# Kernel optimization log

Measured on AMD Instinct MI355X. Metric: run time of the kernel, lower is better.

The kernel has to match this reference:

```python
import jax, jax.numpy as jnp
import numpy as np

D_IN, D, H, NE, NPATCH, B = 768, 512, 4, 2048, 49, 512
DH = D // H


def _match(q, k, w, b):
    # q:[N,Lq,D], k:[N,Lk,D] -> cross-attention of q over k, then linear proj
    s = jnp.einsum('nqd,nkd->nqk', q, k) * (q.shape[-1] ** -0.5)
    a = jax.nn.softmax(s, axis=-1)
    return jnp.einsum('nqk,nkd->nqd', a, k) @ w + b


def _mh_pool(x, query, wq, bq, wk, bk, wv, bv, wo, bo):
    # multi-head attention pooling with 1 learned query -> [N, D]
    N, P, _ = x.shape
    q = (query @ wq + bq).reshape(H, 1, DH)                      # [H,1,dh]
    k = (x @ wk + bk).reshape(N, P, H, DH).transpose(0, 2, 1, 3)  # [N,H,P,dh]
    v = (x @ wv + bv).reshape(N, P, H, DH).transpose(0, 2, 1, 3)
    s = jnp.einsum('hqd,nhkd->nhqk', q, k) * (DH ** -0.5)
    a = jax.nn.softmax(s, axis=-1)
    o = jnp.einsum('nhqk,nhkd->nhqd', a, v).transpose(0, 2, 1, 3).reshape(N, D)
    return o @ wo + bo


def _ln(x, g, b):
    m = jnp.mean(x, -1, keepdims=True)
    v = jnp.var(x, -1, keepdims=True)
    return (x - m) * jax.lax.rsqrt(v + 1e-5) * g + b


def _moe(t, i, gw, gb, tw1, tb1, tw2, tb2, iw1, ib1, iw2, ib2):
    # 2-expert softmax-gated combiner over (text, pooled image) features
    gate = jax.nn.softmax(jnp.concatenate([t, i], -1) @ gw + gb, axis=-1)  # [N,2]
    et = jax.nn.relu(t @ tw1 + tb1) @ tw2 + tb2
    ei = jax.nn.relu(i @ iw1 + ib1) @ iw2 + ib2
    return gate[:, :1] * et + gate[:, 1:] * ei


def setup_inputs():
    key = jax.random.key(0)
    ks = jax.random.split(key, 24)
    g = lambda i, sh, s=0.02: jax.random.normal(ks[i], sh, dtype=jnp.float32) * s
    z = lambda *sh: jnp.zeros(sh, jnp.float32)
    return dict(
        entity_text_cls=g(0, (NE, D_IN), 1.0),
        entity_image_tokens=g(1, (NE, NPATCH, D_IN), 1.0),
        mention_text_cls=g(2, (B, D_IN), 1.0),
        mention_image_tokens=g(3, (B, NPATCH, D_IN), 1.0),
        text_fc_w=g(4, (D_IN, D)), text_fc_b=z(D),
        image_fc_w=g(5, (D_IN, D)), image_fc_b=z(D),
        gate_fc_w=g(6, (D, 1)), gate_fc_b=z(1),
        ln_g=jnp.ones((D,), jnp.float32), ln_b=z(D),
        match_w=g(7, (D, D)), match_b=z(D),
        mh_query=g(8, (1, D)),
        mh_wq=g(9, (D, D)), mh_bq=z(D),
        mh_wk=g(10, (D, D)), mh_bk=z(D),
        mh_wv=g(11, (D, D)), mh_bv=z(D),
        mh_wo=g(12, (D, D)), mh_bo=z(D),
        moe_gw=g(13, (2 * D, 2)), moe_gb=z(2),
        moe_tw1=g(14, (D, D)), moe_tb1=z(D),
        moe_tw2=g(15, (D, D)), moe_tb2=z(D),
        moe_iw1=g(16, (D, D)), moe_ib1=z(D),
        moe_iw2=g(17, (D, D)), moe_ib2=z(D),
    )


def reference(entity_text_cls, entity_image_tokens, mention_text_cls, mention_image_tokens,
              text_fc_w, text_fc_b, image_fc_w, image_fc_b, gate_fc_w, gate_fc_b,
              ln_g, ln_b, match_w, match_b, mh_query,
              mh_wq, mh_bq, mh_wk, mh_bk, mh_wv, mh_bv, mh_wo, mh_bo,
              moe_gw, moe_gb, moe_tw1, moe_tb1, moe_tw2, moe_tb2,
              moe_iw1, moe_ib1, moe_iw2, moe_ib2):
    def side(cls, toks):
        cls_p = cls @ text_fc_w + text_fc_b          # [N,D]
        tok_p = toks @ image_fc_w + image_fc_b       # [N,P,D]
        txt = _match(cls_p[:, None, :], tok_p, match_w, match_b)[:, 0]
        img = _match(tok_p, cls_p[:, None, :], match_w, match_b)
        img = _mh_pool(img, mh_query, mh_wq, mh_bq, mh_wk, mh_bk, mh_wv, mh_bv, mh_wo, mh_bo)
        ctx = _moe(txt, img, moe_gw, moe_gb, moe_tw1, moe_tb1, moe_tw2, moe_tb2,
                   moe_iw1, moe_ib1, moe_iw2, moe_ib2)
        gate = jnp.tanh(cls_p @ gate_fc_w + gate_fc_b)
        return _ln(cls_p * gate + ctx, ln_g, ln_b)

    e_ctx = side(entity_text_cls, entity_image_tokens)   # [NE,D]
    m_ctx = side(mention_text_cls, mention_image_tokens)  # [B,D]
    return m_ctx @ e_ctx.T                                # [B,NE]
```

## Files before the change

### kernel.cpp

```cpp
#include <hip/hip_runtime.h>
#include <hip/hip_bf16.h>
#include <math.h>

namespace {
constexpr int kNE   = 2048;
constexpr int kB    = 512;
constexpr int kDin  = 768;
constexpr int kD    = 512;
constexpr int kP    = 49;
constexpr int kNtot = kNE + kB;
}

typedef __attribute__((ext_vector_type(8))) short bf16x8;
typedef __attribute__((ext_vector_type(4))) float f32x4;

__device__ inline ushort f2bf(float f) {
  unsigned u = __float_as_uint(f);
  return (ushort)((u + 0x7fffu + ((u >> 16) & 1u)) >> 16);
}
__device__ inline void split1(float v, ushort& h, ushort& l) {
  unsigned u = __float_as_uint(v);
  h = (ushort)(u >> 16);
  l = f2bf(v - __uint_as_float(u & 0xFFFF0000u));
}

struct GemmJob {
  const ushort *Ah, *Al;
  const ushort *Bh, *Bl;
  const float* bias;
  float* Cf;
  ushort *Ch, *Cl;
  int M, N, K, relu;
};
struct GemmBatch { GemmJob j[6]; int prefix[7]; };

__global__ __launch_bounds__(256) void gemm_batch(GemmBatch batch) {
  int ji = 0;
  { const int bid = blockIdx.x;
    while (ji < 5 && bid >= batch.prefix[ji + 1]) ++ji; }
  const GemmJob jb = batch.j[ji];
  const int local = blockIdx.x - batch.prefix[ji];
  const int nbx = jb.N >> 6;
  const int by = local / nbx;
  const int bx = local - by * nbx;
  const int row0 = by * 64, col0 = bx * 64;
  const int K = jb.K;
  const int nt = K >> 5;

  __shared__ ushort Ahs[2][64][40], Als[2][64][40];
  __shared__ ushort Bhs[2][64][40], Bls[2][64][40];

  const int tid  = threadIdx.x;
  const int lane = tid & 63;
  const int w    = tid >> 6;
  const int wr   = (w >> 1) * 32;
  const int wc   = (w & 1) * 32;
  const int fr   = lane & 15;
  const int fk   = (lane >> 4) * 8;
  const int sr   = tid >> 2;
  const int sk   = (tid & 3) * 8;

  const ushort* pAh = jb.Ah + (size_t)(row0 + sr) * K + sk;
  const ushort* pAl = jb.Al + (size_t)(row0 + sr) * K + sk;
  const ushort* pBh = jb.Bh + (size_t)(col0 + sr) * K + sk;
  const ushort* pBl = jb.Bl + (size_t)(col0 + sr) * K + sk;

  bf16x8 rAh, rAl, rBh, rBl;
  auto LOAD = [&](int t) {
    const int o = t * 32;
    rAh = *(const bf16x8*)(pAh + o); rAl = *(const bf16x8*)(pAl + o);
    rBh = *(const bf16x8*)(pBh + o); rBl = *(const bf16x8*)(pBl + o);
  };
  auto STORE = [&](int b) {
    *(bf16x8*)&Ahs[b][sr][sk] = rAh; *(bf16x8*)&Als[b][sr][sk] = rAl;
    *(bf16x8*)&Bhs[b][sr][sk] = rBh; *(bf16x8*)&Bls[b][sr][sk] = rBl;
  };

  f32x4 acc[2][2] = {};

  LOAD(0); STORE(0);
  if (nt > 1) LOAD(1);
  __syncthreads();

  for (int t = 0; t < nt; ++t) {
    const int cur = t & 1;
    bf16x8 bh[2], bl[2], ah[2], al[2];
#pragma unroll
    for (int n = 0; n < 2; ++n) {
      bh[n] = *(const bf16x8*)&Bhs[cur][wc + n * 16 + fr][fk];
      bl[n] = *(const bf16x8*)&Bls[cur][wc + n * 16 + fr][fk];
    }
#pragma unroll
    for (int m = 0; m < 2; ++m) {
      ah[m] = *(const bf16x8*)&Ahs[cur][wr + m * 16 + fr][fk];
      al[m] = *(const bf16x8*)&Als[cur][wr + m * 16 + fr][fk];
    }
#pragma unroll
    for (int m = 0; m < 2; ++m)
#pragma unroll
      for (int n = 0; n < 2; ++n) {
        acc[m][n] = __builtin_amdgcn_mfma_f32_16x16x32_bf16(ah[m], bh[n], acc[m][n], 0, 0, 0);
        acc[m][n] = __builtin_amdgcn_mfma_f32_16x16x32_bf16(al[m], bh[n], acc[m][n], 0, 0, 0);
        acc[m][n] = __builtin_amdgcn_mfma_f32_16x16x32_bf16(ah[m], bl[n], acc[m][n], 0, 0, 0);
      }
    if (t + 1 < nt) {
      STORE(cur ^ 1);
      if (t + 2 < nt) LOAD(t + 2);
    }
    __syncthreads();
  }

  const int fq = lane >> 4;
#pragma unroll
  for (int n = 0; n < 2; ++n) {
    const int col = col0 + wc + n * 16 + fr;
    const float bv = jb.bias ? jb.bias[col] : 0.f;
#pragma unroll
    for (int m = 0; m < 2; ++m) {
      const int rbase = row0 + wr + m * 16 + fq * 4;
#pragma unroll
      for (int jj = 0; jj < 4; ++jj) {
        float v = acc[m][n][jj] + bv;
        if (jb.relu) v = fmaxf(v, 0.f);
        const size_t idx = (size_t)(rbase + jj) * jb.N + col;
        if (jb.Cf) jb.Cf[idx] = v;
        if (jb.Ch) { ushort h, l; split1(v, h, l); jb.Ch[idx] = h; jb.Cl[idx] = l; }
      }
    }
  }
}

struct SplitJob { const float* src; ushort* hi; ushort* lo; int n4; };
struct TSJob { const float* src; ushort* hi; ushort* lo; int R, C; };
struct PrepArgs {
  SplitJob s[5];
  TSJob t[7];
  const float *img_b, *match_w, *match_b, *mh_wv, *mh_bv;
  float *bcomb;
  ushort *bt1pad_h, *bt1pad_l;
  int prefix[15];
};

__global__ __launch_bounds__(256) void prep_all(PrepArgs a) {
  int ji = 0;
  { const int bid = blockIdx.x;
    while (ji < 13 && bid >= a.prefix[ji + 1]) ++ji; }
  const int local = blockIdx.x - a.prefix[ji];
  const int t = threadIdx.x;
  __shared__ float tl[32][33];
  __shared__ float rr[4];

  if (ji < 5) {
    const SplitJob jb = a.s[ji];
    const int i = local * 256 + t;
    if (i < jb.n4) {
      float4 v = *(const float4*)&jb.src[(size_t)i * 4];
      ushort4 h, l;
      split1(v.x, h.x, l.x); split1(v.y, h.y, l.y);
      split1(v.z, h.z, l.z); split1(v.w, h.w, l.w);
      *(ushort4*)&jb.hi[(size_t)i * 4] = h;
      *(ushort4*)&jb.lo[(size_t)i * 4] = l;
    }
  } else if (ji < 12) {
    const TSJob jb = a.t[ji - 5];
    const int ntx = jb.C / 32;
    const int r0 = (local / ntx) * 32, c0 = (local % ntx) * 32;
    const int tx = t & 31, ty = t >> 5;
#pragma unroll
    for (int i = 0; i < 32; i += 8)
      tl[ty + i][tx] = jb.src[(size_t)(r0 + ty + i) * jb.C + c0 + tx];
    __syncthreads();
#pragma unroll
    for (int i = 0; i < 32; i += 8) {
      ushort h, l; split1(tl[tx][ty + i], h, l);
      const size_t idx = (size_t)(c0 + ty + i) * jb.R + r0 + tx;
      jb.hi[idx] = h; jb.lo[idx] = l;
    }
  } else {
    const int j = local;
    const float* vec  = (ji == 12) ? a.img_b : a.match_b;
    const float* W    = (ji == 12) ? a.match_w : a.mh_wv;
    const float* badd = (ji == 12) ? a.match_b : a.mh_bv;
    float acc = 0.f;
    for (int k = t; k < kD; k += 256) acc = fmaf(vec[k], W[(size_t)k * kD + j], acc);
    for (int o = 32; o; o >>= 1) acc += __shfl_xor(acc, o);
    if ((t & 63) == 0) rr[t >> 6] = acc;
    __syncthreads();
    if (t == 0) {
      const float v = rr[0] + rr[1] + rr[2] + rr[3] + badd[j];
      if (ji == 12) a.bcomb[j] = v;
      else { ushort h, l; split1(v, h, l); a.bt1pad_h[j] = h; a.bt1pad_l[j] = l; }
    }
  }
}

struct PoolImgArgs {
  GemmJob g; int gemmBlocks;
  const float *ent_toks, *men_toks, *u;
  ushort *wh, *wl;
};

__global__ __launch_bounds__(256) void pool_img(PoolImgArgs a) {
  __shared__ ushort smem[15360];
  __shared__ float sm[4], sl[4];
  const int t = threadIdx.x;
  const int lane = t & 63, wave = t >> 6;

  if ((int)blockIdx.x < a.gemmBlocks) {
    ushort (*Ahs)[40] = (ushort(*)[40])&smem[0];
    ushort (*Als)[40] = (ushort(*)[40])&smem[2560];
    ushort (*Bhs)[40] = (ushort(*)[40])&smem[5120];
    ushort (*Bls)[40] = (ushort(*)[40])&smem[10240];
    const GemmJob jb = a.g;
    const int local = blockIdx.x;
    const int nbx = jb.N >> 7;
    const int by = local / nbx, bx = local - by * nbx;
    const int row0 = by * 64, col0 = bx * 128;
    const int K = jb.K;
    const int w = wave, fr = lane & 15, fk = (lane >> 4) * 8;
    const int sr = t >> 2, sk = (t & 3) * 8;
    f32x4 acc[4][2] = {};
    for (int k0 = 0; k0 < K; k0 += 32) {
      *(bf16x8*)&Ahs[sr][sk] = *(const bf16x8*)&jb.Ah[(size_t)(row0 + sr) * K + k0 + sk];
      *(bf16x8*)&Als[sr][sk] = *(const bf16x8*)&jb.Al[(size_t)(row0 + sr) * K + k0 + sk];
      *(bf16x8*)&Bhs[sr][sk] = *(const bf16x8*)&jb.Bh[(size_t)(col0 + sr) * K + k0 + sk];
      *(bf16x8*)&Bls[sr][sk] = *(const bf16x8*)&jb.Bl[(size_t)(col0 + sr) * K + k0 + sk];
      *(bf16x8*)&Bhs[64 + sr][sk] = *(const bf16x8*)&jb.Bh[(size_t)(col0 + 64 + sr) * K + k0 + sk];
      *(bf16x8*)&Bls[64 + sr][sk] = *(const bf16x8*)&jb.Bl[(size_t)(col0 + 64 + sr) * K + k0 + sk];
      __syncthreads();
      bf16x8 bh[2], bl[2];
#pragma unroll
      for (int n = 0; n < 2; ++n) {
        bh[n] = *(const bf16x8*)&Bhs[w * 32 + n * 16 + fr][fk];
        bl[n] = *(const bf16x8*)&Bls[w * 32 + n * 16 + fr][fk];
      }
#pragma unroll
      for (int m = 0; m < 4; ++m) {
        bf16x8 ah = *(const bf16x8*)&Ahs[m * 16 + fr][fk];
        bf16x8 al = *(const bf16x8*)&Als[m * 16 + fr][fk];
#pragma unroll
        for (int n = 0; n < 2; ++n) {
          acc[m][n] = __builtin_amdgcn_mfma_f32_16x16x32_bf16(ah, bh[n], acc[m][n], 0, 0, 0);
          acc[m][n] = __builtin_amdgcn_mfma_f32_16x16x32_bf16(al, bh[n], acc[m][n], 0, 0, 0);
          acc[m][n] = __builtin_amdgcn_mfma_f32_16x16x32_bf16(ah, bl[n], acc[m][n], 0, 0, 0);
        }
      }
      __syncthreads();
    }
    const int fq = lane >> 4;
#pragma unroll
    for (int n = 0; n < 2; ++n) {
      const int col = col0 + w * 32 + n * 16 + fr;
      const float bv = jb.bias ? jb.bias[col] : 0.f;
#pragma unroll
      for (int m = 0; m < 4; ++m) {
        const int rbase = row0 + m * 16 + fq * 4;
#pragma unroll
        for (int jj = 0; jj < 4; ++jj) {
          float v = acc[m][n][jj] + bv;
          if (jb.relu) v = fmaxf(v, 0.f);
          const size_t idx = (size_t)(rbase + jj) * jb.N + col;
          if (jb.Cf) jb.Cf[idx] = v;
          if (jb.Ch) { ushort h, l; split1(v, h, l); jb.Ch[idx] = h; jb.Cl[idx] = l; }
        }
      }
    }
    return;
  }

  float* sacc = (float*)smem;
  const int n = blockIdx.x - a.gemmBlocks;
  const float* toks = (n < kNE) ? a.ent_toks + (size_t)n * kP * kDin
                                : a.men_toks + (size_t)(n - kNE) * kP * kDin;
  const float* un = a.u + (size_t)n * kDin;
  const float scale = 0.044194173824159216f;

  f32x4 ureg[3];
#pragma unroll
  for (int r = 0; r < 3; ++r) ureg[r] = *(const f32x4*)&un[4 * lane + 256 * r];

  float m = -INFINITY, l = 0.f;
  f32x4 acc[3] = {};

  for (int p = wave; p < kP; p += 4) {
    const float* tp = toks + (size_t)p * kDin;
    f32x4 tv[3];
#pragma unroll
    for (int r = 0; r < 3; ++r) tv[r] = *(const f32x4*)&tp[4 * lane + 256 * r];
    float d = 0.f;
#pragma unroll
    for (int r = 0; r < 3; ++r)
#pragma unroll
      for (int i = 0; i < 4; ++i) d = fmaf(tv[r][i], ureg[r][i], d);
    for (int o = 32; o; o >>= 1) d += __shfl_xor(d, o);
    const float s = d * scale;
    const float mn = fmaxf(m, s);
    const float c = __expf(m - mn);
    const float e = __expf(s - mn);
    l = l * c + e;
#pragma unroll
    for (int r = 0; r < 3; ++r) acc[r] = acc[r] * c + tv[r] * e;
    m = mn;
  }

#pragma unroll
  for (int r = 0; r < 3; ++r)
    *(f32x4*)&sacc[wave * kDin + 4 * lane + 256 * r] = acc[r];
  if (lane == 0) { sm[wave] = m; sl[wave] = l; }
  __syncthreads();

  const float M = fmaxf(fmaxf(sm[0], sm[1]), fmaxf(sm[2], sm[3]));
  const float c0 = __expf(sm[0] - M), c1 = __expf(sm[1] - M);
  const float c2 = __expf(sm[2] - M), c3 = __expf(sm[3] - M);
  const float inv = 1.f / (sl[0] * c0 + sl[1] * c1 + sl[2] * c2 + sl[3] * c3);

  const size_t base = (size_t)n * kDin;
#pragma unroll
  for (int r = 0; r < 3; ++r) {
    const int dd = t + r * 256;
    const float v = (sacc[0 * kDin + dd] * c0 + sacc[1 * kDin + dd] * c1 +
                     sacc[2 * kDin + dd] * c2 + sacc[3 * kDin + dd] * c3) * inv;
    ushort h, lo; split1(v, h, lo);
    a.wh[base + dd] = h; a.wl[base + dd] = lo;
  }
}

__global__ __launch_bounds__(256) void finalize_ln(
    const float* __restrict__ cls_p, const float* __restrict__ et,
    const float* __restrict__ ei, const float* __restrict__ txt,
    const float* __restrict__ img,
    const float* __restrict__ gw, const float* __restrict__ gb,
    const float* __restrict__ gfw, const float* __restrict__ gfb,
    const float* __restrict__ lng, const float* __restrict__ lnb,
    ushort* __restrict__ ch, ushort* __restrict__ cl) {
  const int n = blockIdx.x;
  const int t = threadIdx.x;
  const int lane = t & 63, wave = t >> 6;
  const size_t base = (size_t)n * kD;
  const float c0 = cls_p[base + t], c1 = cls_p[base + 256 + t];

  const float t0 = txt[base + t], t1 = txt[base + 256 + t];
  const float i0 = img[base + t], i1 = img[base + 256 + t];
  float d  = fmaf(c0, gfw[t], c1 * gfw[t + 256]);
  float p0 = fmaf(t0, gw[t * 2 + 0], fmaf(t1, gw[(t + 256) * 2 + 0],
             fmaf(i0, gw[(512 + t) * 2 + 0], i1 * gw[(768 + t) * 2 + 0])));
  float p1 = fmaf(t0, gw[t * 2 + 1], fmaf(t1, gw[(t + 256) * 2 + 1],
             fmaf(i0, gw[(512 + t) * 2 + 1], i1 * gw[(768 + t) * 2 + 1])));
  for (int o = 32; o; o >>= 1) {
    d += __shfl_xor(d, o); p0 += __shfl_xor(p0, o); p1 += __shfl_xor(p1, o);
  }
  __shared__ float rd[4], r0[4], r1[4];
  __shared__ float gtb, g0b, g1b;
  if (lane == 0) { rd[wave] = d; r0[wave] = p0; r1[wave] = p1; }
  __syncthreads();
  if (t == 0) {
    gtb = tanhf(rd[0] + rd[1] + rd[2] + rd[3] + gfb[0]);
    const float l0 = r0[0] + r0[1] + r0[2] + r0[3] + gb[0];
    const float l1 = r1[0] + r1[1] + r1[2] + r1[3] + gb[1];
    const float mm = fmaxf(l0, l1);
    const float e0 = __expf(l0 - mm), e1 = __expf(l1 - mm);
    const float inv = 1.f / (e0 + e1);
    g0b = e0 * inv; g1b = e1 * inv;
  }
  __syncthreads();
  const float gt = gtb, g0 = g0b, g1 = g1b;

  const float y0 = c0 * gt + g0 * et[base + t]       + g1 * ei[base + t];
  const float y1 = c1 * gt + g0 * et[base + 256 + t] + g1 * ei[base + 256 + t];

  float s = y0 + y1, ss = fmaf(y0, y0, y1 * y1);
  for (int o = 32; o; o >>= 1) { s += __shfl_xor(s, o); ss += __shfl_xor(ss, o); }
  __shared__ float rsum[4], rssq[4];
  __shared__ float mb, ivb;
  if (lane == 0) { rsum[wave] = s; rssq[wave] = ss; }
  __syncthreads();
  if (t == 0) {
    const float S  = rsum[0] + rsum[1] + rsum[2] + rsum[3];
    const float SS = rssq[0] + rssq[1] + rssq[2] + rssq[3];
    const float mm = S / (float)kD;
    const float v  = SS / (float)kD - mm * mm;
    mb = mm; ivb = rsqrtf(v + 1e-5f);
  }
  __syncthreads();
  const float mm = mb, iv = ivb;
  ushort h, l;
  split1((y0 - mm) * iv * lng[t] + lnb[t], h, l);
  ch[base + t] = h; cl[base + t] = l;
  split1((y1 - mm) * iv * lng[t + 256] + lnb[t + 256], h, l);
  ch[base + 256 + t] = h; cl[base + 256 + t] = l;
}

extern "C" void kernel_launch(void* const* d_in, const int* in_sizes, int n_in,
                              void* d_out, int out_size, void* d_ws, size_t ws_size,
                              hipStream_t stream) {
  const float* ent_cls  = (const float*)d_in[0];
  const float* ent_tok  = (const float*)d_in[1];
  const float* men_cls  = (const float*)d_in[2];
  const float* men_tok  = (const float*)d_in[3];
  const float* text_w   = (const float*)d_in[4];
  const float* text_b   = (const float*)d_in[5];
  const float* img_w    = (const float*)d_in[6];
  const float* img_b    = (const float*)d_in[7];
  const float* gate_w   = (const float*)d_in[8];
  const float* gate_b   = (const float*)d_in[9];
  const float* ln_g     = (const float*)d_in[10];
  const float* ln_b     = (const float*)d_in[11];
  const float* match_w  = (const float*)d_in[12];
  const float* match_b  = (const float*)d_in[13];
  const float* mh_wv    = (const float*)d_in[19];
  const float* mh_bv    = (const float*)d_in[20];
  const float* mh_wo    = (const float*)d_in[21];
  const float* mh_bo    = (const float*)d_in[22];
  const float* moe_gw   = (const float*)d_in[23];
  const float* moe_gb   = (const float*)d_in[24];
  const float* moe_tw1  = (const float*)d_in[25];
  const float* moe_tb1  = (const float*)d_in[26];
  const float* moe_tw2  = (const float*)d_in[27];
  const float* moe_tb2  = (const float*)d_in[28];
  const float* moe_iw1  = (const float*)d_in[29];
  const float* moe_ib1  = (const float*)d_in[30];
  const float* moe_iw2  = (const float*)d_in[31];
  const float* moe_ib2  = (const float*)d_in[32];
  (void)ws_size; (void)n_in; (void)in_sizes; (void)out_size;

  char* base = (char*)d_ws;
  size_t off = 0;
  auto allocB = [&](size_t bytes) -> char* {
    char* p = base + off; off = (off + bytes + 255) & ~(size_t)255; return p;
  };
  auto allocF = [&](size_t n) { return (float*)allocB(n * 4); };
  auto allocU = [&](size_t n) { return (ushort*)allocB(n * 2); };

  float* clsp_f = allocF((size_t)kNtot * kD);
  float* u_f    = allocF((size_t)kNtot * kDin);
  float* txt_f  = allocF((size_t)kNtot * kD);
  float* img_f  = allocF((size_t)kNtot * kD);
  float* et_f   = allocF((size_t)kNtot * kD);
  float* ei_f   = allocF((size_t)kNtot * kD);
  float* bcomb  = allocF(kD);
  float* bimg_pad = allocF((size_t)64 * kD);
  auto pair = [&](size_t n, ushort*& h, ushort*& l) { h = allocU(n); l = allocU(n); };
  ushort *ent_h,*ent_l,*men_h,*men_l,*imgw_h,*imgw_l,*matw_h,*matw_l,*mhwv_h,*mhwv_l;
  pair((size_t)kNE * kDin, ent_h, ent_l);
  pair((size_t)kB * kDin, men_h, men_l);
  pair((size_t)kDin * kD, imgw_h, imgw_l);
  pair((size_t)kD * kD, matw_h, matw_l);
  pair((size_t)kD * kD, mhwv_h, mhwv_l);
  ushort *textWT_h,*textWT_l,*matchWT_h,*matchWT_l,*mhWoT_h,*mhWoT_l;
  ushort *tw1T_h,*tw1T_l,*tw2T_h,*tw2T_l,*iw1T_h,*iw1T_l,*iw2T_h,*iw2T_l;
  pair((size_t)kD * kDin, textWT_h, textWT_l);
  pair((size_t)kD * kD, matchWT_h, matchWT_l);
  pair((size_t)kD * kD, mhWoT_h, mhWoT_l);
  pair((size_t)kD * kD, tw1T_h, tw1T_l);
  pair((size_t)kD * kD, tw2T_h, tw2T_l);
  pair((size_t)kD * kD, iw1T_h, iw1T_l);
  pair((size_t)kD * kD, iw2T_h, iw2T_l);
  ushort *clsp_h,*clsp_l,*U_h,*U_l,*WcombT_h,*WcombT_l,*WimgT_h,*WimgT_l;
  ushort *bt1pad_h,*bt1pad_l;
  pair((size_t)kNtot * kD, clsp_h, clsp_l);
  pair((size_t)kD * kD, U_h, U_l);
  pair((size_t)kD * kDin, WcombT_h, WcombT_l);
  pair((size_t)kD * kD, WimgT_h, WimgT_l);
  pair((size_t)64 * kD, bt1pad_h, bt1pad_l);
  ushort *ws_h,*ws_l,*txt_h,*txt_l,*img_h,*img_l,*ht_h,*ht_l,*hi_h,*hi_l,*ctx_h,*ctx_l;
  pair((size_t)kNtot * kDin, ws_h, ws_l);
  pair((size_t)kNtot * kD, txt_h, txt_l);
  pair((size_t)kNtot * kD, img_h, img_l);
  pair((size_t)kNtot * kD, ht_h, ht_l);
  pair((size_t)kNtot * kD, hi_h, hi_l);
  pair((size_t)kNtot * kD, ctx_h, ctx_l);

  auto nblk = [](const GemmJob& j) { return (j.M / 64) * (j.N / 64); };
  auto launch_batch = [&](int njobs, GemmJob j0, GemmJob j1 = {}, GemmJob j2 = {},
                          GemmJob j3 = {}, GemmJob j4 = {}, GemmJob j5 = {}) {
    GemmBatch b{};
    b.j[0] = j0; b.j[1] = j1; b.j[2] = j2; b.j[3] = j3; b.j[4] = j4; b.j[5] = j5;
    b.prefix[0] = 0;
    for (int i = 0; i < 6; ++i)
      b.prefix[i + 1] = b.prefix[i] + (i < njobs ? nblk(b.j[i]) : 0);
    hipLaunchKernelGGL(gemm_batch, dim3(b.prefix[njobs]), 256, 0, stream, b);
  };

  PrepArgs pa{};
  pa.s[0] = { ent_cls, ent_h, ent_l, kNE * kDin / 4 };
  pa.s[1] = { men_cls, men_h, men_l, kB * kDin / 4 };
  pa.s[2] = { img_w,   imgw_h, imgw_l, kDin * kD / 4 };
  pa.s[3] = { match_w, matw_h, matw_l, kD * kD / 4 };
  pa.s[4] = { mh_wv,   mhwv_h, mhwv_l, kD * kD / 4 };
  pa.t[0] = { text_w,  textWT_h,  textWT_l,  kDin, kD };
  pa.t[1] = { match_w, matchWT_h, matchWT_l, kD,   kD };
  pa.t[2] = { mh_wo,   mhWoT_h,   mhWoT_l,   kD,   kD };
  pa.t[3] = { moe_tw1, tw1T_h,    tw1T_l,    kD,   kD };
  pa.t[4] = { moe_tw2, tw2T_h,    tw2T_l,    kD,   kD };
  pa.t[5] = { moe_iw1, iw1T_h,    iw1T_l,    kD,   kD };
  pa.t[6] = { moe_iw2, iw2T_h,    iw2T_l,    kD,   kD };
  pa.img_b = img_b; pa.match_w = match_w; pa.match_b = match_b;
  pa.mh_wv = mh_wv; pa.mh_bv = mh_bv;
  pa.bcomb = bcomb; pa.bt1pad_h = bt1pad_h; pa.bt1pad_l = bt1pad_l;
  {
    int pfx = 0; int c = 0;
    pa.prefix[c++] = 0;
    for (int i = 0; i < 5; ++i) { pfx += (pa.s[i].n4 + 255) / 256; pa.prefix[c++] = pfx; }
    for (int i = 0; i < 7; ++i) { pfx += (pa.t[i].R / 32) * (pa.t[i].C / 32); pa.prefix[c++] = pfx; }
    for (int i = 0; i < 2; ++i) { pfx += kD; pa.prefix[c++] = pfx; }
    hipLaunchKernelGGL(prep_all, dim3(pfx), 256, 0, stream, pa);
  }

  launch_batch(5,
    GemmJob{ ent_h, ent_l, textWT_h, textWT_l, text_b,
             clsp_f, clsp_h, clsp_l, kNE, kD, kDin, 0 },
    GemmJob{ men_h, men_l, textWT_h, textWT_l, text_b,
             clsp_f + (size_t)kNE * kD, clsp_h + (size_t)kNE * kD,
             clsp_l + (size_t)kNE * kD, kB, kD, kDin, 0 },
    GemmJob{ matchWT_h, matchWT_l, imgw_h, imgw_l, nullptr,
             nullptr, WcombT_h, WcombT_l, kD, kDin, kD, 0 },
    GemmJob{ mhWoT_h, mhWoT_l, mhwv_h, mhwv_l, nullptr,
             nullptr, U_h, U_l, kD, kD, kD, 0 },
    GemmJob{ bt1pad_h, bt1pad_l, mhWoT_h, mhWoT_l, mh_bo,
             bimg_pad, nullptr, nullptr, 64, kD, kD, 0 });

  launch_batch(2,
    GemmJob{ clsp_h, clsp_l, imgw_h, imgw_l, nullptr,
             u_f, nullptr, nullptr, kNtot, kDin, kD, 0 },
    GemmJob{ U_h, U_l, matw_h, matw_l, nullptr,
             nullptr, WimgT_h, WimgT_l, kD, kD, kD, 0 });

  {
    PoolImgArgs pia{};
    pia.g = GemmJob{ clsp_h, clsp_l, WimgT_h, WimgT_l, bimg_pad,
                     img_f, img_h, img_l, kNtot, kD, kD, 0 };
    pia.gemmBlocks = (kNtot / 64) * (kD / 128);
    pia.ent_toks = ent_tok; pia.men_toks = men_tok; pia.u = u_f;
    pia.wh = ws_h; pia.wl = ws_l;
    hipLaunchKernelGGL(pool_img, dim3(pia.gemmBlocks + kNtot), 256, 0, stream, pia);
  }

  launch_batch(1,
    GemmJob{ ws_h, ws_l, WcombT_h, WcombT_l, bcomb,
             txt_f, txt_h, txt_l, kNtot, kD, kDin, 0 });

  launch_batch(2,
    GemmJob{ txt_h, txt_l, tw1T_h, tw1T_l, moe_tb1,
             nullptr, ht_h, ht_l, kNtot, kD, kD, 1 },
    GemmJob{ img_h, img_l, iw1T_h, iw1T_l, moe_ib1,
             nullptr, hi_h, hi_l, kNtot, kD, kD, 1 });

  launch_batch(2,
    GemmJob{ ht_h, ht_l, tw2T_h, tw2T_l, moe_tb2,
             et_f, nullptr, nullptr, kNtot, kD, kD, 0 },
    GemmJob{ hi_h, hi_l, iw2T_h, iw2T_l, moe_ib2,
             ei_f, nullptr, nullptr, kNtot, kD, kD, 0 });

  hipLaunchKernelGGL(finalize_ln, dim3(kNtot), 256, 0, stream,
                     clsp_f, et_f, ei_f, txt_f, img_f,
                     moe_gw, moe_gb, gate_w, gate_b, ln_g, ln_b, ctx_h, ctx_l);

  launch_batch(1,
    GemmJob{ ctx_h + (size_t)kNE * kD, ctx_l + (size_t)kNE * kD,
             ctx_h, ctx_l, nullptr,
             (float*)d_out, nullptr, nullptr, kB, kNE, kD, 0 });
}
```

Measured before the change: 219.2 us.

## Shrink pool_img GEMM tile to 64x64 and rebalance MoE GEMM launch batches

The GEMM portion of pool_img moves from 64x128 tiles to 64x64 tiles with a 2x2 wave layout. This doubles the number of GEMM blocks and reduces shared memory per block, which should improve occupancy and load balance next to the pooling blocks. The image-expert first layer now runs in the same batch as the text combine GEMM, so the independent MoE branches are regrouped into the same number of launches with a different dependency order. Each block now reloads the A tile, so A operand traffic doubles in exchange for more parallelism.

```diff
diff --git a/kernel.cpp b/kernel.cpp
--- a/kernel.cpp
+++ b/kernel.cpp
@@ -201,7 +201,7 @@
 };
 
 __global__ __launch_bounds__(256) void pool_img(PoolImgArgs a) {
-  __shared__ ushort smem[15360];
+  __shared__ ushort smem[10240];
   __shared__ float sm[4], sl[4];
   const int t = threadIdx.x;
   const int lane = t & 63, wave = t >> 6;
@@ -210,51 +210,52 @@
     ushort (*Ahs)[40] = (ushort(*)[40])&smem[0];
     ushort (*Als)[40] = (ushort(*)[40])&smem[2560];
     ushort (*Bhs)[40] = (ushort(*)[40])&smem[5120];
-    ushort (*Bls)[40] = (ushort(*)[40])&smem[10240];
+    ushort (*Bls)[40] = (ushort(*)[40])&smem[7680];
     const GemmJob jb = a.g;
     const int local = blockIdx.x;
-    const int nbx = jb.N >> 7;
+    const int nbx = jb.N >> 6;
     const int by = local / nbx, bx = local - by * nbx;
-    const int row0 = by * 64, col0 = bx * 128;
+    const int row0 = by * 64, col0 = bx * 64;
     const int K = jb.K;
-    const int w = wave, fr = lane & 15, fk = (lane >> 4) * 8;
+    const int wr = (wave >> 1) * 32, wc = (wave & 1) * 32;
+    const int fr = lane & 15, fk = (lane >> 4) * 8;
     const int sr = t >> 2, sk = (t & 3) * 8;
-    f32x4 acc[4][2] = {};
+    f32x4 acc[2][2] = {};
     for (int k0 = 0; k0 < K; k0 += 32) {
       *(bf16x8*)&Ahs[sr][sk] = *(const bf16x8*)&jb.Ah[(size_t)(row0 + sr) * K + k0 + sk];
       *(bf16x8*)&Als[sr][sk] = *(const bf16x8*)&jb.Al[(size_t)(row0 + sr) * K + k0 + sk];
       *(bf16x8*)&Bhs[sr][sk] = *(const bf16x8*)&jb.Bh[(size_t)(col0 + sr) * K + k0 + sk];
       *(bf16x8*)&Bls[sr][sk] = *(const bf16x8*)&jb.Bl[(size_t)(col0 + sr) * K + k0 + sk];
-      *(bf16x8*)&Bhs[64 + sr][sk] = *(const bf16x8*)&jb.Bh[(size_t)(col0 + 64 + sr) * K + k0 + sk];
-      *(bf16x8*)&Bls[64 + sr][sk] = *(const bf16x8*)&jb.Bl[(size_t)(col0 + 64 + sr) * K + k0 + sk];
       __syncthreads();
-      bf16x8 bh[2], bl[2];
+      bf16x8 bh[2], bl[2], ah[2], al[2];
 #pragma unroll
       for (int n = 0; n < 2; ++n) {
-        bh[n] = *(const bf16x8*)&Bhs[w * 32 + n * 16 + fr][fk];
-        bl[n] = *(const bf16x8*)&Bls[w * 32 + n * 16 + fr][fk];
+        bh[n] = *(const bf16x8*)&Bhs[wc + n * 16 + fr][fk];
+        bl[n] = *(const bf16x8*)&Bls[wc + n * 16 + fr][fk];
       }
 #pragma unroll
-      for (int m = 0; m < 4; ++m) {
-        bf16x8 ah = *(const bf16x8*)&Ahs[m * 16 + fr][fk];
-        bf16x8 al = *(const bf16x8*)&Als[m * 16 + fr][fk];
+      for (int m = 0; m < 2; ++m) {
+        ah[m] = *(const bf16x8*)&Ahs[wr + m * 16 + fr][fk];
+        al[m] = *(const bf16x8*)&Als[wr + m * 16 + fr][fk];
+      }
+#pragma unroll
+      for (int m = 0; m < 2; ++m)
 #pragma unroll
         for (int n = 0; n < 2; ++n) {
-          acc[m][n] = __builtin_amdgcn_mfma_f32_16x16x32_bf16(ah, bh[n], acc[m][n], 0, 0, 0);
-          acc[m][n] = __builtin_amdgcn_mfma_f32_16x16x32_bf16(al, bh[n], acc[m][n], 0, 0, 0);
-          acc[m][n] = __builtin_amdgcn_mfma_f32_16x16x32_bf16(ah, bl[n], acc[m][n], 0, 0, 0);
+          acc[m][n] = __builtin_amdgcn_mfma_f32_16x16x32_bf16(ah[m], bh[n], acc[m][n], 0, 0, 0);
+          acc[m][n] = __builtin_amdgcn_mfma_f32_16x16x32_bf16(al[m], bh[n], acc[m][n], 0, 0, 0);
+          acc[m][n] = __builtin_amdgcn_mfma_f32_16x16x32_bf16(ah[m], bl[n], acc[m][n], 0, 0, 0);
         }
-      }
       __syncthreads();
     }
     const int fq = lane >> 4;
 #pragma unroll
     for (int n = 0; n < 2; ++n) {
-      const int col = col0 + w * 32 + n * 16 + fr;
+      const int col = col0 + wc + n * 16 + fr;
       const float bv = jb.bias ? jb.bias[col] : 0.f;
 #pragma unroll
-      for (int m = 0; m < 4; ++m) {
-        const int rbase = row0 + m * 16 + fq * 4;
+      for (int m = 0; m < 2; ++m) {
+        const int rbase = row0 + wr + m * 16 + fq * 4;
 #pragma unroll
         for (int jj = 0; jj < 4; ++jj) {
           float v = acc[m][n][jj] + bv;
@@ -529,27 +530,27 @@
     PoolImgArgs pia{};
     pia.g = GemmJob{ clsp_h, clsp_l, WimgT_h, WimgT_l, bimg_pad,
                      img_f, img_h, img_l, kNtot, kD, kD, 0 };
-    pia.gemmBlocks = (kNtot / 64) * (kD / 128);
+    pia.gemmBlocks = (kNtot / 64) * (kD / 64);
     pia.ent_toks = ent_tok; pia.men_toks = men_tok; pia.u = u_f;
     pia.wh = ws_h; pia.wl = ws_l;
     hipLaunchKernelGGL(pool_img, dim3(pia.gemmBlocks + kNtot), 256, 0, stream, pia);
   }
 
-  launch_batch(1,
+  launch_batch(2,
     GemmJob{ ws_h, ws_l, WcombT_h, WcombT_l, bcomb,
-             txt_f, txt_h, txt_l, kNtot, kD, kDin, 0 });
+             txt_f, txt_h, txt_l, kNtot, kD, kDin, 0 },
+    GemmJob{ img_h, img_l, iw1T_h, iw1T_l, moe_ib1,
+             nullptr, hi_h, hi_l, kNtot, kD, kD, 1 });
 
   launch_batch(2,
     GemmJob{ txt_h, txt_l, tw1T_h, tw1T_l, moe_tb1,
              nullptr, ht_h, ht_l, kNtot, kD, kD, 1 },
-    GemmJob{ img_h, img_l, iw1T_h, iw1T_l, moe_ib1,
-             nullptr, hi_h, hi_l, kNtot, kD, kD, 1 });
-
-  launch_batch(2,
-    GemmJob{ ht_h, ht_l, tw2T_h, tw2T_l, moe_tb2,
-             et_f, nullptr, nullptr, kNtot, kD, kD, 0 },
     GemmJob{ hi_h, hi_l, iw2T_h, iw2T_l, moe_ib2,
              ei_f, nullptr, nullptr, kNtot, kD, kD, 0 });
+
+  launch_batch(1,
+    GemmJob{ ht_h, ht_l, tw2T_h, tw2T_l, moe_tb2,
+             et_f, nullptr, nullptr, kNtot, kD, kD, 0 });
 
   hipLaunchKernelGGL(finalize_ln, dim3(kNtot), 256, 0, stream,
                      clsp_f, et_f, ei_f, txt_f, img_f,
```

New measurement: 220.7 us. Within noise of the previous version (+0.7%).
